# Performance work log

Hardware: AMD Instinct MI355X
Metric: run time of the kernel (lower is better)

## Reference

```python
import jax, jax.numpy as jnp
import numpy as np

N_NODES = 50000
N_EDGES = 800000
NODE_DIM = 32
EDGE_DIM = 16
HID = 64
MSG_HID = 128
NUM_GRAPHS = 512
NUM_MP = 3
S2S_STEPS = 6


def _lin(k, fan_in, fan_out):
    # torch Linear default init: U(-1/sqrt(fan_in), 1/sqrt(fan_in))
    bound = 1.0 / np.sqrt(fan_in)
    kw, kb = jax.random.split(k)
    W = jax.random.uniform(kw, (fan_in, fan_out), jnp.float32, -bound, bound)
    b = jax.random.uniform(kb, (fan_out,), jnp.float32, -bound, bound)
    return W, b


def setup_inputs() -> dict:
    key = jax.random.key(0)
    ks = jax.random.split(key, 16)
    x_feat = jax.random.normal(ks[0], (N_NODES, NODE_DIM), jnp.float32)
    edge_index = jax.random.randint(ks[1], (2, N_EDGES), 0, N_NODES)
    edge_attr = jax.random.normal(ks[2], (N_EDGES, EDGE_DIM), jnp.float32)
    batch = jnp.sort(jax.random.randint(ks[3], (N_NODES,), 0, NUM_GRAPHS))
    W_emb, b_emb = _lin(ks[4], NODE_DIM, HID)
    W_m1, b_m1 = _lin(ks[5], 2 * HID + EDGE_DIM, MSG_HID)
    W_m2, b_m2 = _lin(ks[6], MSG_HID, HID)
    bnd = 1.0 / np.sqrt(HID)
    gru_W_ih = jax.random.uniform(ks[7], (3 * HID, HID), jnp.float32, -bnd, bnd)
    gru_W_hh = jax.random.uniform(ks[8], (3 * HID, HID), jnp.float32, -bnd, bnd)
    gru_b_ih = jax.random.uniform(ks[9], (3 * HID,), jnp.float32, -bnd, bnd)
    gru_b_hh = jax.random.uniform(ks[9], (3 * HID,), jnp.float32, -bnd, bnd)
    lstm_W_ih = jax.random.uniform(ks[10], (4 * HID, 2 * HID), jnp.float32, -bnd, bnd)
    lstm_W_hh = jax.random.uniform(ks[11], (4 * HID, HID), jnp.float32, -bnd, bnd)
    lstm_b_ih = jax.random.uniform(ks[12], (4 * HID,), jnp.float32, -bnd, bnd)
    lstm_b_hh = jax.random.uniform(ks[12], (4 * HID,), jnp.float32, -bnd, bnd)
    W_r1, b_r1 = _lin(ks[13], 2 * HID, HID)
    W_r2, b_r2 = _lin(ks[14], HID, 1)
    return dict(x_feat=x_feat, edge_index=edge_index, edge_attr=edge_attr, batch=batch,
                W_emb=W_emb, b_emb=b_emb, W_m1=W_m1, b_m1=b_m1, W_m2=W_m2, b_m2=b_m2,
                gru_W_ih=gru_W_ih, gru_W_hh=gru_W_hh, gru_b_ih=gru_b_ih, gru_b_hh=gru_b_hh,
                lstm_W_ih=lstm_W_ih, lstm_W_hh=lstm_W_hh, lstm_b_ih=lstm_b_ih, lstm_b_hh=lstm_b_hh,
                W_r1=W_r1, b_r1=b_r1, W_r2=W_r2, b_r2=b_r2)


def reference(x_feat, edge_index, edge_attr, batch,
              W_emb, b_emb, W_m1, b_m1, W_m2, b_m2,
              gru_W_ih, gru_W_hh, gru_b_ih, gru_b_hh,
              lstm_W_ih, lstm_W_hh, lstm_b_ih, lstm_b_hh,
              W_r1, b_r1, W_r2, b_r2):
    src, dst = edge_index[0], edge_index[1]
    x = x_feat @ W_emb + b_emb  # [N, HID]
    h = x  # GRU hidden state (seq_len=1 GRU)
    for _ in range(NUM_MP):
        # message: cat([x_i (target), x_j (source), edge_attr]) -> MLP -> scatter-add to target
        mi = jnp.concatenate([x[dst], x[src], edge_attr], axis=-1)  # [E, 2H+Ed]
        msg = jnp.maximum(mi @ W_m1 + b_m1, 0.0) @ W_m2 + b_m2  # [E, H]
        m = jax.ops.segment_sum(msg, dst, num_segments=N_NODES)  # [N, H]
        # torch GRU cell, gate order (r, z, n)
        gi = m @ gru_W_ih.T + gru_b_ih
        gh = h @ gru_W_hh.T + gru_b_hh
        ir, iz, i_n = jnp.split(gi, 3, axis=-1)
        hr, hz, h_n = jnp.split(gh, 3, axis=-1)
        r = jax.nn.sigmoid(ir + hr)
        z = jax.nn.sigmoid(iz + hz)
        n = jnp.tanh(i_n + r * h_n)
        h = (1.0 - z) * n + z * h
        x = h
    # Set2Set pooling
    qh = jnp.zeros((NUM_GRAPHS, HID), x.dtype)
    qc = jnp.zeros((NUM_GRAPHS, HID), x.dtype)
    q_star = jnp.zeros((NUM_GRAPHS, 2 * HID), x.dtype)
    for _ in range(S2S_STEPS):
        # torch LSTM cell, gate order (i, f, g, o)
        g = q_star @ lstm_W_ih.T + lstm_b_ih + qh @ lstm_W_hh.T + lstm_b_hh
        gi_, gf, gg, go = jnp.split(g, 4, axis=-1)
        qc = jax.nn.sigmoid(gf) * qc + jax.nn.sigmoid(gi_) * jnp.tanh(gg)
        qh = jax.nn.sigmoid(go) * jnp.tanh(qc)
        e = jnp.sum(x * qh[batch], axis=-1)  # [N]
        emax = jax.ops.segment_max(e, batch, num_segments=NUM_GRAPHS)
        a = jnp.exp(e - emax[batch])
        asum = jax.ops.segment_sum(a, batch, num_segments=NUM_GRAPHS)
        a = a / asum[batch]  # segment softmax
        rvec = jax.ops.segment_sum(a[:, None] * x, batch, num_segments=NUM_GRAPHS)  # [B, H]
        q_star = jnp.concatenate([qh, rvec], axis=-1)
    out = jnp.maximum(q_star @ W_r1 + b_r1, 0.0) @ W_r2 + b_r2
    return out
```

## Files before the change

kernel.cpp:

```cpp
#include <hip/hip_runtime.h>
#include <hip/hip_bf16.h>

#define HID 64
#define MSG 128
#define NDIM 32
#define EDIM 16
#define NG 512
#define SCAP 192

typedef unsigned short u16;
typedef unsigned int u32;
typedef _Float16 h8 __attribute__((ext_vector_type(8)));
typedef _Float16 h4 __attribute__((ext_vector_type(4)));
typedef _Float16 h2 __attribute__((ext_vector_type(2)));

__device__ __forceinline__ float sigm(float x){return 1.0f/(1.0f+expf(-x));}
__device__ __forceinline__ int rfl(int x){return __builtin_amdgcn_readfirstlane(x);}
__device__ __forceinline__ u32 pkh(float a, float b){
    union { h2 h; u32 u; } v; v.h[0] = (_Float16)a; v.h[1] = (_Float16)b; return v.u;
}
__device__ __forceinline__ h2 pk2h(float a, float b){
    union { __fp16 __attribute__((ext_vector_type(2))) r; h2 h; } v;
    v.r = __builtin_amdgcn_cvt_pkrtz(a, b);
    return v.h;
}
__device__ __forceinline__ float fdot2_(h2 a, u32 w, float c){
    union { u32 u; h2 h; } v; v.u = w;
    return __builtin_amdgcn_fdot2(a, v.h, c, false);
}

__global__ void k_hist(const int* __restrict__ idx, int n, int* __restrict__ cnt) {
    int i = blockIdx.x * blockDim.x + threadIdx.x;
    int stride = gridDim.x * blockDim.x;
    for (; i < n; i += stride) atomicAdd(&cnt[idx[i]], 1);
}

__global__ void k_scanA(const int* __restrict__ in, int* __restrict__ out,
                        int* __restrict__ bsum, int n) {
    __shared__ int sh[1024];
    int i = blockIdx.x * 1024 + threadIdx.x;
    int v = (i < n) ? in[i] : 0;
    sh[threadIdx.x] = v;
    __syncthreads();
    for (int off = 1; off < 1024; off <<= 1) {
        int t = (threadIdx.x >= off) ? sh[threadIdx.x - off] : 0;
        __syncthreads();
        sh[threadIdx.x] += t;
        __syncthreads();
    }
    if (i < n) out[i] = sh[threadIdx.x] - v;
    if (threadIdx.x == 1023) bsum[blockIdx.x] = sh[1023];
}
__global__ void k_scanB(const int* __restrict__ bsum, int* __restrict__ boff, int nb) {
    if (threadIdx.x == 0) {
        int r = 0;
        for (int b = 0; b < nb; b++) { boff[b] = r; r += bsum[b]; }
        boff[nb] = r;
    }
}
__global__ void k_scanC(int* __restrict__ out, const int* __restrict__ boff, int n, int nb) {
    int i = blockIdx.x * blockDim.x + threadIdx.x;
    if (i < n) out[i] += boff[i >> 10];
    else if (i == n) out[n] = boff[nb];
}

__global__ void k_gptr(const int* __restrict__ batch, int N, int* __restrict__ gptr) {
    int g = blockIdx.x * blockDim.x + threadIdx.x;
    if (g > NG) return;
    int lo = 0, hi = N;
    while (lo < hi) { int mid = (lo + hi) >> 1; if (batch[mid] < g) lo = mid + 1; else hi = mid; }
    gptr[g] = lo;
}

__global__ void k_scatter(const int* __restrict__ src, const int* __restrict__ dst,
                          const float* __restrict__ ea, int n,
                          const int* __restrict__ ptr, int* __restrict__ cursor,
                          int* __restrict__ slist, _Float16* __restrict__ eap) {
    int i = blockIdx.x * blockDim.x + threadIdx.x;
    int stride = gridDim.x * blockDim.x;
    for (; i < n; i += stride) {
        int d = dst[i];
        int pos = ptr[d] + atomicAdd(&cursor[d], 1);
        slist[pos] = src[i];
        const float* s = ea + (size_t)i * EDIM;
        float4 a = *(const float4*)s, b = *(const float4*)(s + 4);
        float4 c = *(const float4*)(s + 8), d4 = *(const float4*)(s + 12);
        h8 o0, o1;
        o0[0]=(_Float16)a.x; o0[1]=(_Float16)a.y; o0[2]=(_Float16)a.z; o0[3]=(_Float16)a.w;
        o0[4]=(_Float16)b.x; o0[5]=(_Float16)b.y; o0[6]=(_Float16)b.z; o0[7]=(_Float16)b.w;
        o1[0]=(_Float16)c.x; o1[1]=(_Float16)c.y; o1[2]=(_Float16)c.z; o1[3]=(_Float16)c.w;
        o1[4]=(_Float16)d4.x; o1[5]=(_Float16)d4.y; o1[6]=(_Float16)d4.z; o1[7]=(_Float16)d4.w;
        h8* dp = (h8*)(eap + (size_t)pos * EDIM);
        dp[0] = o0; dp[1] = o1;
    }
}

__global__ void k_fuse(const float* __restrict__ Wih, const float* __restrict__ Whh,
                       const float* __restrict__ W2, const float* __restrict__ bm2,
                       uint4* __restrict__ gGA, uint2* __restrict__ gGB,
                       uint4* __restrict__ gUA, uint2* __restrict__ gUB,
                       float* __restrict__ gbb) {
    int t = blockIdx.x * blockDim.x + threadIdx.x;
    if (t < 2048) {
        int k4 = t >> 6, c = t & 63;
        float G[3][4];
#pragma unroll
        for (int g = 0; g < 3; g++)
#pragma unroll
            for (int kk = 0; kk < 4; kk++) {
                int j = 4 * k4 + kk;
                const float* w2r = W2 + (size_t)j * 64;
                const float* wir = Wih + (size_t)(g * 64 + c) * 64;
                float s = 0.f;
                for (int k = 0; k < 64; k++) s += w2r[k] * wir[k];
                G[g][kk] = s;
            }
        uint4 A; uint2 B;
        A.x = pkh(G[0][0], G[0][1]); A.y = pkh(G[1][0], G[1][1]);
        A.z = pkh(G[2][0], G[2][1]); A.w = pkh(G[0][2], G[0][3]);
        B.x = pkh(G[1][2], G[1][3]); B.y = pkh(G[2][2], G[2][3]);
        gGA[t] = A; gGB[t] = B;
    } else if (t < 3072) {
        int u = t - 2048;
        int k4 = u >> 6, c = u & 63;
        float U[3][4];
#pragma unroll
        for (int g = 0; g < 3; g++)
#pragma unroll
            for (int kk = 0; kk < 4; kk++)
                U[g][kk] = Whh[(size_t)(g * 64 + c) * 64 + 4 * k4 + kk];
        uint4 A; uint2 B;
        A.x = pkh(U[0][0], U[0][1]); A.y = pkh(U[1][0], U[1][1]);
        A.z = pkh(U[2][0], U[2][1]); A.w = pkh(U[0][2], U[0][3]);
        B.x = pkh(U[1][2], U[1][3]); B.y = pkh(U[2][2], U[2][3]);
        gUA[u] = A; gUB[u] = B;
    } else if (t < 3072 + 192) {
        int cg = t - 3072;
        const float* wir = Wih + (size_t)cg * 64;
        float s = 0.f;
        for (int k = 0; k < 64; k++) s += bm2[k] * wir[k];
        gbb[cg] = s;
    }
}

__global__ void k_packl(const float* __restrict__ lWih, const float* __restrict__ lWhh,
                        float* __restrict__ WT1, float* __restrict__ WT2) {
    int t = blockIdx.x * blockDim.x + threadIdx.x;
    if (t < 256 * 128) { int g = t >> 7, k = t & 127; WT1[k * 256 + g] = lWih[g * 128 + k]; }
    if (t < 256 * 64)  { int g = t >> 6, k = t & 63;  WT2[k * 256 + g] = lWhh[g * 64 + k]; }
}

__global__ void k_embed(const float* __restrict__ xf, const float* __restrict__ We,
                        const float* __restrict__ be, float* __restrict__ xh, int N) {
    __shared__ float Wl[NDIM * HID];
    for (int t = threadIdx.x; t < NDIM * HID; t += blockDim.x) Wl[t] = We[t];
    __syncthreads();
    int total = N * HID;
    int stride = gridDim.x * blockDim.x;
    for (int idx = blockIdx.x * blockDim.x + threadIdx.x; idx < total; idx += stride) {
        int n = idx >> 6, c = idx & 63;
        const float* xr = xf + n * NDIM;
        float acc = be[c];
#pragma unroll
        for (int k = 0; k < NDIM; k++) acc += xr[k] * Wl[k * HID + c];
        xh[idx] = acc;
    }
}

__global__ void __launch_bounds__(512)
k_prep(const float* __restrict__ xh, const float* __restrict__ Wm1,
       const float* __restrict__ bm1, float* __restrict__ Hb,
       _Float16* __restrict__ PsH, int N) {
    __shared__ float Wl[64 * 256];
    for (int t = threadIdx.x; t < 64 * 256; t += 512) {
        int k = t >> 8, cc = t & 255;
        Wl[t] = (cc < 128) ? Wm1[k * 128 + cc] : Wm1[(64 + k) * 128 + (cc - 128)];
    }
    __syncthreads();
    int wv = threadIdx.x >> 6, lane = threadIdx.x & 63;
    int cc = lane * 4;
    float4 bias;
    if (lane < 32) bias = *(const float4*)&bm1[cc];
    else bias = make_float4(0.f, 0.f, 0.f, 0.f);
    int ngroups = (N + 7) >> 3;
    for (int g = blockIdx.x * 8 + wv; g < ngroups; g += gridDim.x * 8) {
        int base = rfl(g) * 8;
        const float* xp[8];
#pragma unroll
        for (int t = 0; t < 8; t++) {
            int d = base + t; if (d > N - 1) d = N - 1;
            xp[t] = xh + (size_t)d * 64;
        }
        float4 acc[8];
#pragma unroll
        for (int t = 0; t < 8; t++) acc[t] = bias;
#pragma unroll 2
        for (int k4 = 0; k4 < 16; k4++) {
            int k = k4 * 4;
            float4 xv4[8];
#pragma unroll
            for (int t = 0; t < 8; t++) xv4[t] = *(const float4*)&xp[t][k];
#pragma unroll
            for (int kk = 0; kk < 4; kk++) {
                float4 w = *(const float4*)&Wl[(k + kk) * 256 + cc];
#pragma unroll
                for (int t = 0; t < 8; t++) {
                    float xv = kk == 0 ? xv4[t].x : kk == 1 ? xv4[t].y : kk == 2 ? xv4[t].z : xv4[t].w;
                    acc[t].x += xv * w.x; acc[t].y += xv * w.y;
                    acc[t].z += xv * w.z; acc[t].w += xv * w.w;
                }
            }
        }
#pragma unroll
        for (int t = 0; t < 8; t++) {
            int d = base + t;
            if (d < N) {
                if (lane < 32) *(float4*)&Hb[(size_t)d * 128 + cc] = acc[t];
                else {
                    h4 o;
                    o[0] = (_Float16)acc[t].x; o[1] = (_Float16)acc[t].y;
                    o[2] = (_Float16)acc[t].z; o[3] = (_Float16)acc[t].w;
                    *(h4*)&PsH[(size_t)d * 128 + (cc - 128)] = o;
                }
            }
        }
    }
}

__global__ void __launch_bounds__(256)
k_edge(const _Float16* __restrict__ PsH, const _Float16* __restrict__ eap,
       const float* __restrict__ Wm1, const int* __restrict__ ptr,
       const int* __restrict__ slist, float* __restrict__ Hb, int N) {
    int c = threadIdx.x & 127;
    int half = threadIdx.x >> 7;
    h2 wh[8];
#pragma unroll
    for (int k = 0; k < 8; k++) {
        h2 t;
        t[0] = (_Float16)Wm1[128 * 128 + (2 * k) * 128 + c];
        t[1] = (_Float16)Wm1[128 * 128 + (2 * k + 1) * 128 + c];
        wh[k] = t;
    }
    for (int dd = blockIdx.x * 2 + half; dd < N; dd += gridDim.x * 2) {
        int d = rfl(dd);
        float pd = Hb[(size_t)d * 128 + c];
        int eb = rfl(ptr[d]), ee = rfl(ptr[d + 1]);
        const int* sp = slist + eb;
        const _Float16* ep = eap + (size_t)eb * EDIM;
        int ne = ee - eb;
        float acc = 0.f;
        int i = 0;
        for (; i + 8 <= ne; i += 8) {
            int ns[8];
#pragma unroll
            for (int j = 0; j < 8; j++) ns[j] = rfl(sp[i + j]);
            float pv[8];
#pragma unroll
            for (int j = 0; j < 8; j++) pv[j] = (float)PsH[(size_t)ns[j] * 128 + c];
#pragma unroll
            for (int j = 0; j < 8; j++) {
                union { uint4 u; h2 h[4]; } A, B;
                A.u = *(const uint4*)(ep + (size_t)(i + j) * EDIM);
                B.u = *(const uint4*)(ep + (size_t)(i + j) * EDIM + 8);
                float pe = 0.f;
#pragma unroll
                for (int k = 0; k < 4; k++) pe = __builtin_amdgcn_fdot2(A.h[k], wh[k], pe, false);
#pragma unroll
                for (int k = 0; k < 4; k++) pe = __builtin_amdgcn_fdot2(B.h[k], wh[4 + k], pe, false);
                acc += fmaxf(pd + pv[j] + pe, 0.f);
            }
        }
        for (; i < ne; i++) {
            int n0 = rfl(sp[i]);
            float pv = (float)PsH[(size_t)n0 * 128 + c];
            union { uint4 u; h2 h[4]; } A, B;
            A.u = *(const uint4*)(ep + (size_t)i * EDIM);
            B.u = *(const uint4*)(ep + (size_t)i * EDIM + 8);
            float pe = 0.f;
#pragma unroll
            for (int k = 0; k < 4; k++) pe = __builtin_amdgcn_fdot2(A.h[k], wh[k], pe, false);
#pragma unroll
            for (int k = 0; k < 4; k++) pe = __builtin_amdgcn_fdot2(B.h[k], wh[4 + k], pe, false);
            acc += fmaxf(pd + pv + pe, 0.f);
        }
        Hb[(size_t)d * 128 + c] = acc;
    }
}

__global__ void __launch_bounds__(1024)
k_node(const float* __restrict__ H, const uint4* __restrict__ gGA, const uint2* __restrict__ gGB,
       const uint4* __restrict__ gUA, const uint2* __restrict__ gUB,
       const float* __restrict__ gbb, const float* __restrict__ bih, const float* __restrict__ bhh,
       const int* __restrict__ ptr, const float* __restrict__ xin, float* __restrict__ xout, int N) {
    extern __shared__ char smem[];
    uint4* GA = (uint4*)smem;
    uint2* GB = (uint2*)(smem + 32768);
    uint4* UA = (uint4*)(smem + 49152);
    uint2* UB = (uint2*)(smem + 65536);
    for (int t = threadIdx.x; t < 2048; t += 1024) { GA[t] = gGA[t]; GB[t] = gGB[t]; }
    for (int t = threadIdx.x; t < 1024; t += 1024) { UA[t] = gUA[t]; UB[t] = gUB[t]; }
    __syncthreads();
    int wv = threadIdx.x >> 6, lane = threadIdx.x & 63;
    float gbr = gbb[lane], gbz = gbb[64 + lane], gbn = gbb[128 + lane];
    float br = bih[lane], bz = bih[64 + lane], bn = bih[128 + lane];
    float cr = bhh[lane], cz = bhh[64 + lane], cn = bhh[128 + lane];
    int ngroups = (N + 3) >> 2;
    for (int g = blockIdx.x * 16 + wv; g < ngroups; g += gridDim.x * 16) {
        int base = rfl(g) * 4;
        const float* hp[4]; const float* xp[4]; float deg[4];
#pragma unroll
        for (int t = 0; t < 4; t++) {
            int d = base + t; if (d > N - 1) d = N - 1;
            hp[t] = H + (size_t)d * 128;
            xp[t] = xin + (size_t)d * 64;
            deg[t] = (float)(ptr[d + 1] - ptr[d]);
        }
        float gr[4], gz[4], gn[4];
#pragma unroll
        for (int t = 0; t < 4; t++) {
            gr[t] = br + deg[t] * gbr;
            gz[t] = bz + deg[t] * gbz;
            gn[t] = bn + deg[t] * gbn;
        }
#pragma unroll 2
        for (int k4 = 0; k4 < 32; k4++) {
            uint4 wa = GA[k4 * 64 + lane];
            uint2 wb = GB[k4 * 64 + lane];
#pragma unroll
            for (int t = 0; t < 4; t++) {
                float4 hx = *(const float4*)&hp[t][k4 * 4];
                h2 a01 = pk2h(hx.x, hx.y), a23 = pk2h(hx.z, hx.w);
                gr[t] = fdot2_(a01, wa.x, gr[t]); gz[t] = fdot2_(a01, wa.y, gz[t]);
                gn[t] = fdot2_(a01, wa.z, gn[t]);
                gr[t] = fdot2_(a23, wa.w, gr[t]); gz[t] = fdot2_(a23, wb.x, gz[t]);
                gn[t] = fdot2_(a23, wb.y, gn[t]);
            }
        }
        float hr[4], hz[4], hn[4], hv[4];
#pragma unroll
        for (int t = 0; t < 4; t++) { hr[t] = cr; hz[t] = cz; hn[t] = cn; hv[t] = xp[t][lane]; }
#pragma unroll 2
        for (int k4 = 0; k4 < 16; k4++) {
            uint4 wa = UA[k4 * 64 + lane];
            uint2 wb = UB[k4 * 64 + lane];
#pragma unroll
            for (int t = 0; t < 4; t++) {
                float4 hx = *(const float4*)&xp[t][k4 * 4];
                h2 a01 = pk2h(hx.x, hx.y), a23 = pk2h(hx.z, hx.w);
                hr[t] = fdot2_(a01, wa.x, hr[t]); hz[t] = fdot2_(a01, wa.y, hz[t]);
                hn[t] = fdot2_(a01, wa.z, hn[t]);
                hr[t] = fdot2_(a23, wa.w, hr[t]); hz[t] = fdot2_(a23, wb.x, hz[t]);
                hn[t] = fdot2_(a23, wb.y, hn[t]);
            }
        }
#pragma unroll
        for (int t = 0; t < 4; t++) {
            int d = base + t;
            if (d < N) {
                float r = sigm(gr[t] + hr[t]);
                float z = sigm(gz[t] + hz[t]);
                float nn = tanhf(gn[t] + r * hn[t]);
                xout[(size_t)d * 64 + lane] = (1.f - z) * nn + z * hv[t];
            }
        }
    }
}

__global__ void __launch_bounds__(1024)
k_s2s(const float* __restrict__ xh, const int* __restrict__ gptr,
      const float* __restrict__ WT1, const float* __restrict__ WT2,
      const float* __restrict__ lbih, const float* __restrict__ lbhh,
      const float* __restrict__ Wr1, const float* __restrict__ br1,
      const float* __restrict__ Wr2, const float* __restrict__ br2,
      float* __restrict__ out) {
    int b = blockIdx.x, tid = threadIdx.x;
    __shared__ float xl[SCAP * 64];
    __shared__ float qs[128], qhl[64], qcs[64], g[256], red[16], asums[16], rvs[1024];
    int start = gptr[b], end = gptr[b + 1];
    int seg = end - start;
    bool uselds = (seg <= SCAP);
    if (uselds) {
        int tot = seg * 64;
        for (int t = tid; t < tot; t += 1024) xl[t] = xh[(size_t)start * 64 + t];
    }
    if (tid < 128) qs[tid] = 0.f;
    if (tid < 64) { qhl[tid] = 0.f; qcs[tid] = 0.f; }
    __syncthreads();
    int grp = tid >> 6, lane = tid & 63;
    int gate = tid & 255, part = tid >> 8;
    for (int s = 0; s < 6; s++) {
        {
            float acc = 0.f;
            int k0 = part * 32;
#pragma unroll 8
            for (int k = k0; k < k0 + 32; k++) acc += qs[k] * WT1[k * 256 + gate];
            int k1 = part * 16;
#pragma unroll 8
            for (int k = k1; k < k1 + 16; k++) acc += qhl[k] * WT2[k * 256 + gate];
            rvs[tid] = acc;
        }
        __syncthreads();
        if (tid < 256) g[tid] = lbih[tid] + lbhh[tid] + rvs[tid] + rvs[256 + tid] + rvs[512 + tid] + rvs[768 + tid];
        __syncthreads();
        if (tid < 64) {
            float ig = sigm(g[tid]), fg = sigm(g[64 + tid]);
            float gg = tanhf(g[128 + tid]), og = sigm(g[192 + tid]);
            float c = fg * qcs[tid] + ig * gg;
            float h = og * tanhf(c);
            qcs[tid] = c; qhl[tid] = h; qs[tid] = h;
        }
        __syncthreads();
        float qv = qhl[lane];
        float mloc = -3.4e38f, asl = 0.f, rv = 0.f;
        for (int n = grp; n < seg; n += 16) {
            float xv = uselds ? xl[n * 64 + lane] : xh[(size_t)(start + n) * 64 + lane];
            float p = xv * qv;
#pragma unroll
            for (int off = 32; off > 0; off >>= 1) p += __shfl_xor(p, off);
            float mnew = fmaxf(mloc, p);
            float corr = expf(mloc - mnew);
            float a = expf(p - mnew);
            asl = asl * corr + a;
            rv = rv * corr + a * xv;
            mloc = mnew;
        }
        if (lane == 0) red[grp] = mloc;
        __syncthreads();
        float gmax = red[0];
#pragma unroll
        for (int j = 1; j < 16; j++) gmax = fmaxf(gmax, red[j]);
        float sc = expf(mloc - gmax);
        rvs[tid] = rv * sc;
        if (lane == 0) asums[grp] = asl * sc;
        __syncthreads();
        if (tid < 64) {
            float rt = 0.f, at = 0.f;
#pragma unroll
            for (int j = 0; j < 16; j++) { rt += rvs[tid + 64 * j]; at += asums[j]; }
            qs[64 + tid] = (at > 0.f) ? rt / at : 0.f;
        }
        __syncthreads();
    }
    if (tid < 64) {
        float a2 = br1[tid];
#pragma unroll 8
        for (int k = 0; k < 128; k++) a2 += qs[k] * Wr1[k * 64 + tid];
        a2 = fmaxf(a2, 0.f);
        float v = a2 * Wr2[tid];
#pragma unroll
        for (int off = 32; off > 0; off >>= 1) v += __shfl_xor(v, off);
        if (tid == 0) out[b] = v + br2[0];
    }
}

extern "C" void kernel_launch(void* const* d_in, const int* in_sizes, int n_in,
                              void* d_out, int out_size, void* d_ws, size_t ws_size,
                              hipStream_t stream) {
    const float* x_feat = (const float*)d_in[0];
    const int*   ei     = (const int*)d_in[1];
    const float* eattr  = (const float*)d_in[2];
    const int*   batch  = (const int*)d_in[3];
    const float* W_emb  = (const float*)d_in[4];
    const float* b_emb  = (const float*)d_in[5];
    const float* W_m1   = (const float*)d_in[6];
    const float* b_m1   = (const float*)d_in[7];
    const float* W_m2   = (const float*)d_in[8];
    const float* b_m2   = (const float*)d_in[9];
    const float* gWih   = (const float*)d_in[10];
    const float* gWhh   = (const float*)d_in[11];
    const float* gbih   = (const float*)d_in[12];
    const float* gbhh   = (const float*)d_in[13];
    const float* lWih   = (const float*)d_in[14];
    const float* lWhh   = (const float*)d_in[15];
    const float* lbih   = (const float*)d_in[16];
    const float* lbhh   = (const float*)d_in[17];
    const float* Wr1    = (const float*)d_in[18];
    const float* br1    = (const float*)d_in[19];
    const float* Wr2    = (const float*)d_in[20];
    const float* br2    = (const float*)d_in[21];

    int N = in_sizes[0] / NDIM;
    int E = in_sizes[1] / 2;

    char* w = (char*)d_ws;
    auto alloc = [&](size_t b) { char* p = w; w += (b + 511) & ~(size_t)511; return p; };
    float*     xh    = (float*)alloc((size_t)N * 64 * 4);
    float*     xh2   = (float*)alloc((size_t)N * 64 * 4);
    _Float16*  PsH   = (_Float16*)alloc((size_t)N * 128 * 2);
    float*     Hb    = (float*)alloc((size_t)N * 128 * 4);
    int*       ptr   = (int*)alloc((size_t)(N + 1) * 4);
    int*       slist = (int*)alloc((size_t)E * 4);
    _Float16*  eap   = (_Float16*)alloc((size_t)E * EDIM * 2);
    uint4*     gGA   = (uint4*)alloc((size_t)2048 * 16);
    uint2*     gGB   = (uint2*)alloc((size_t)2048 * 8);
    uint4*     gUA   = (uint4*)alloc((size_t)1024 * 16);
    uint2*     gUB   = (uint2*)alloc((size_t)1024 * 8);
    float*     gbb   = (float*)alloc((size_t)192 * 4);
    float*     WT1   = (float*)alloc((size_t)128 * 256 * 4);
    float*     WT2   = (float*)alloc((size_t)64 * 256 * 4);
    int*       gptr  = (int*)alloc((size_t)(NG + 1) * 4);
    int*       bsum  = (int*)alloc(128 * 4);
    int*       boff  = (int*)alloc(128 * 4);
    char* z0 = w;
    int*       cnt    = (int*)alloc((size_t)N * 4);
    int*       cursor = (int*)alloc((size_t)N * 4);
    char* z0e = w;

    hipMemsetAsync(z0, 0, (size_t)(z0e - z0), stream);

    hipError_t attr_err = hipFuncSetAttribute((const void*)k_node,
        hipFuncAttributeMaxDynamicSharedMemorySize, 73728);
    (void)attr_err;

    int NB = (N + 1023) / 1024;
    k_hist<<<1024, 256, 0, stream>>>(ei + E, E, cnt);
    k_scanA<<<NB, 1024, 0, stream>>>(cnt, ptr, bsum, N);
    k_scanB<<<1, 64, 0, stream>>>(bsum, boff, NB);
    k_scanC<<<(N + 256) / 256, 256, 0, stream>>>(ptr, boff, N, NB);
    k_gptr<<<3, 256, 0, stream>>>(batch, N, gptr);
    k_scatter<<<3125, 256, 0, stream>>>(ei, ei + E, eattr, E, ptr, cursor, slist, eap);
    k_fuse<<<13, 256, 0, stream>>>(gWih, gWhh, W_m2, b_m2, gGA, gGB, gUA, gUB, gbb);
    k_packl<<<128, 256, 0, stream>>>(lWih, lWhh, WT1, WT2);

    k_embed<<<2048, 256, 0, stream>>>(x_feat, W_emb, b_emb, xh, N);

    float* xa = xh;
    float* xb = xh2;
    for (int r = 0; r < 3; r++) {
        k_prep<<<196, 512, 0, stream>>>(xa, W_m1, b_m1, Hb, PsH, N);
        k_edge<<<4096, 256, 0, stream>>>(PsH, eap, W_m1, ptr, slist, Hb, N);
        k_node<<<256, 1024, 73728, stream>>>(Hb, gGA, gGB, gUA, gUB, gbb, gbih, gbhh,
                                             ptr, xa, xb, N);
        float* t = xa; xa = xb; xb = t;
    }
    k_s2s<<<NG, 1024, 0, stream>>>(xa, gptr, WT1, WT2, lbih, lbhh,
                                   Wr1, br1, Wr2, br2, (float*)d_out);
}
```

Before: 926.4 us.

## Store edge aggregates and node state in fp16 for GRU node kernel

After: 857.3 us. 1.08x faster.

```diff
diff --git a/kernel.cpp b/kernel.cpp
--- a/kernel.cpp
+++ b/kernel.cpp
@@ -19,11 +19,7 @@
 __device__ __forceinline__ u32 pkh(float a, float b){
     union { h2 h; u32 u; } v; v.h[0] = (_Float16)a; v.h[1] = (_Float16)b; return v.u;
 }
-__device__ __forceinline__ h2 pk2h(float a, float b){
-    union { __fp16 __attribute__((ext_vector_type(2))) r; h2 h; } v;
-    v.r = __builtin_amdgcn_cvt_pkrtz(a, b);
-    return v.h;
-}
+__device__ __forceinline__ h2 bh2(u32 u){ union{u32 v; h2 h;} x; x.v=u; return x.h; }
 __device__ __forceinline__ float fdot2_(h2 a, u32 w, float c){
     union { u32 u; h2 h; } v; v.u = w;
     return __builtin_amdgcn_fdot2(a, v.h, c, false);
@@ -151,7 +147,8 @@
 }
 
 __global__ void k_embed(const float* __restrict__ xf, const float* __restrict__ We,
-                        const float* __restrict__ be, float* __restrict__ xh, int N) {
+                        const float* __restrict__ be, float* __restrict__ xh,
+                        _Float16* __restrict__ xh16, int N) {
     __shared__ float Wl[NDIM * HID];
     for (int t = threadIdx.x; t < NDIM * HID; t += blockDim.x) Wl[t] = We[t];
     __syncthreads();
@@ -164,6 +161,7 @@
 #pragma unroll
         for (int k = 0; k < NDIM; k++) acc += xr[k] * Wl[k * HID + c];
         xh[idx] = acc;
+        xh16[idx] = (_Float16)acc;
     }
 }
 
@@ -230,7 +228,8 @@
 __global__ void __launch_bounds__(256)
 k_edge(const _Float16* __restrict__ PsH, const _Float16* __restrict__ eap,
        const float* __restrict__ Wm1, const int* __restrict__ ptr,
-       const int* __restrict__ slist, float* __restrict__ Hb, int N) {
+       const int* __restrict__ slist, const float* __restrict__ Pd,
+       _Float16* __restrict__ Hh, int N) {
     int c = threadIdx.x & 127;
     int half = threadIdx.x >> 7;
     h2 wh[8];
@@ -243,22 +242,42 @@
     }
     for (int dd = blockIdx.x * 2 + half; dd < N; dd += gridDim.x * 2) {
         int d = rfl(dd);
-        float pd = Hb[(size_t)d * 128 + c];
+        float pd = Pd[(size_t)d * 128 + c];
         int eb = rfl(ptr[d]), ee = rfl(ptr[d + 1]);
         const int* sp = slist + eb;
         const _Float16* ep = eap + (size_t)eb * EDIM;
         int ne = ee - eb;
         float acc = 0.f;
         int i = 0;
-        for (; i + 8 <= ne; i += 8) {
-            int ns[8];
-#pragma unroll
-            for (int j = 0; j < 8; j++) ns[j] = rfl(sp[i + j]);
-            float pv[8];
-#pragma unroll
-            for (int j = 0; j < 8; j++) pv[j] = (float)PsH[(size_t)ns[j] * 128 + c];
-#pragma unroll
-            for (int j = 0; j < 8; j++) {
+        for (; i + 16 <= ne; i += 16) {
+            int ns[16];
+#pragma unroll
+            for (int j = 0; j < 16; j++) ns[j] = rfl(sp[i + j]);
+            float pv[16];
+#pragma unroll
+            for (int j = 0; j < 16; j++) pv[j] = (float)PsH[(size_t)ns[j] * 128 + c];
+#pragma unroll
+            for (int j = 0; j < 16; j++) {
+                union { uint4 u; h2 h[4]; } A, B;
+                A.u = *(const uint4*)(ep + (size_t)(i + j) * EDIM);
+                B.u = *(const uint4*)(ep + (size_t)(i + j) * EDIM + 8);
+                float pe = 0.f;
+#pragma unroll
+                for (int k = 0; k < 4; k++) pe = __builtin_amdgcn_fdot2(A.h[k], wh[k], pe, false);
+#pragma unroll
+                for (int k = 0; k < 4; k++) pe = __builtin_amdgcn_fdot2(B.h[k], wh[4 + k], pe, false);
+                acc += fmaxf(pd + pv[j] + pe, 0.f);
+            }
+        }
+        for (; i + 4 <= ne; i += 4) {
+            int ns[4];
+#pragma unroll
+            for (int j = 0; j < 4; j++) ns[j] = rfl(sp[i + j]);
+            float pv[4];
+#pragma unroll
+            for (int j = 0; j < 4; j++) pv[j] = (float)PsH[(size_t)ns[j] * 128 + c];
+#pragma unroll
+            for (int j = 0; j < 4; j++) {
                 union { uint4 u; h2 h[4]; } A, B;
                 A.u = *(const uint4*)(ep + (size_t)(i + j) * EDIM);
                 B.u = *(const uint4*)(ep + (size_t)(i + j) * EDIM + 8);
@@ -283,15 +302,17 @@
             for (int k = 0; k < 4; k++) pe = __builtin_amdgcn_fdot2(B.h[k], wh[4 + k], pe, false);
             acc += fmaxf(pd + pv + pe, 0.f);
         }
-        Hb[(size_t)d * 128 + c] = acc;
+        Hh[(size_t)d * 128 + c] = (_Float16)acc;
     }
 }
 
 __global__ void __launch_bounds__(1024)
-k_node(const float* __restrict__ H, const uint4* __restrict__ gGA, const uint2* __restrict__ gGB,
+k_node(const _Float16* __restrict__ Hh, const uint4* __restrict__ gGA, const uint2* __restrict__ gGB,
        const uint4* __restrict__ gUA, const uint2* __restrict__ gUB,
        const float* __restrict__ gbb, const float* __restrict__ bih, const float* __restrict__ bhh,
-       const int* __restrict__ ptr, const float* __restrict__ xin, float* __restrict__ xout, int N) {
+       const int* __restrict__ ptr, const float* __restrict__ xin,
+       const _Float16* __restrict__ xin16, float* __restrict__ xout,
+       _Float16* __restrict__ xout16, int N) {
     extern __shared__ char smem[];
     uint4* GA = (uint4*)smem;
     uint2* GB = (uint2*)(smem + 32768);
@@ -307,11 +328,12 @@
     int ngroups = (N + 3) >> 2;
     for (int g = blockIdx.x * 16 + wv; g < ngroups; g += gridDim.x * 16) {
         int base = rfl(g) * 4;
-        const float* hp[4]; const float* xp[4]; float deg[4];
+        const _Float16* hp16[4]; const _Float16* xp16[4]; const float* xp[4]; float deg[4];
 #pragma unroll
         for (int t = 0; t < 4; t++) {
             int d = base + t; if (d > N - 1) d = N - 1;
-            hp[t] = H + (size_t)d * 128;
+            hp16[t] = Hh + (size_t)d * 128;
+            xp16[t] = xin16 + (size_t)d * 64;
             xp[t] = xin + (size_t)d * 64;
             deg[t] = (float)(ptr[d + 1] - ptr[d]);
         }
@@ -323,34 +345,44 @@
             gn[t] = bn + deg[t] * gbn;
         }
 #pragma unroll 2
-        for (int k4 = 0; k4 < 32; k4++) {
-            uint4 wa = GA[k4 * 64 + lane];
-            uint2 wb = GB[k4 * 64 + lane];
+        for (int k8 = 0; k8 < 16; k8++) {
+            uint4 wa0 = GA[(2 * k8) * 64 + lane];
+            uint2 wb0 = GB[(2 * k8) * 64 + lane];
+            uint4 wa1 = GA[(2 * k8 + 1) * 64 + lane];
+            uint2 wb1 = GB[(2 * k8 + 1) * 64 + lane];
 #pragma unroll
             for (int t = 0; t < 4; t++) {
-                float4 hx = *(const float4*)&hp[t][k4 * 4];
-                h2 a01 = pk2h(hx.x, hx.y), a23 = pk2h(hx.z, hx.w);
-                gr[t] = fdot2_(a01, wa.x, gr[t]); gz[t] = fdot2_(a01, wa.y, gz[t]);
-                gn[t] = fdot2_(a01, wa.z, gn[t]);
-                gr[t] = fdot2_(a23, wa.w, gr[t]); gz[t] = fdot2_(a23, wb.x, gz[t]);
-                gn[t] = fdot2_(a23, wb.y, gn[t]);
+                uint4 a = *(const uint4*)(hp16[t] + k8 * 8);
+                gr[t] = fdot2_(bh2(a.x), wa0.x, gr[t]); gz[t] = fdot2_(bh2(a.x), wa0.y, gz[t]);
+                gn[t] = fdot2_(bh2(a.x), wa0.z, gn[t]);
+                gr[t] = fdot2_(bh2(a.y), wa0.w, gr[t]); gz[t] = fdot2_(bh2(a.y), wb0.x, gz[t]);
+                gn[t] = fdot2_(bh2(a.y), wb0.y, gn[t]);
+                gr[t] = fdot2_(bh2(a.z), wa1.x, gr[t]); gz[t] = fdot2_(bh2(a.z), wa1.y, gz[t]);
+                gn[t] = fdot2_(bh2(a.z), wa1.z, gn[t]);
+                gr[t] = fdot2_(bh2(a.w), wa1.w, gr[t]); gz[t] = fdot2_(bh2(a.w), wb1.x, gz[t]);
+                gn[t] = fdot2_(bh2(a.w), wb1.y, gn[t]);
             }
         }
         float hr[4], hz[4], hn[4], hv[4];
 #pragma unroll
         for (int t = 0; t < 4; t++) { hr[t] = cr; hz[t] = cz; hn[t] = cn; hv[t] = xp[t][lane]; }
 #pragma unroll 2
-        for (int k4 = 0; k4 < 16; k4++) {
-            uint4 wa = UA[k4 * 64 + lane];
-            uint2 wb = UB[k4 * 64 + lane];
+        for (int k8 = 0; k8 < 8; k8++) {
+            uint4 wa0 = UA[(2 * k8) * 64 + lane];
+            uint2 wb0 = UB[(2 * k8) * 64 + lane];
+            uint4 wa1 = UA[(2 * k8 + 1) * 64 + lane];
+            uint2 wb1 = UB[(2 * k8 + 1) * 64 + lane];
 #pragma unroll
             for (int t = 0; t < 4; t++) {
-                float4 hx = *(const float4*)&xp[t][k4 * 4];
-                h2 a01 = pk2h(hx.x, hx.y), a23 = pk2h(hx.z, hx.w);
-                hr[t] = fdot2_(a01, wa.x, hr[t]); hz[t] = fdot2_(a01, wa.y, hz[t]);
-                hn[t] = fdot2_(a01, wa.z, hn[t]);
-                hr[t] = fdot2_(a23, wa.w, hr[t]); hz[t] = fdot2_(a23, wb.x, hz[t]);
-                hn[t] = fdot2_(a23, wb.y, hn[t]);
+                uint4 a = *(const uint4*)(xp16[t] + k8 * 8);
+                hr[t] = fdot2_(bh2(a.x), wa0.x, hr[t]); hz[t] = fdot2_(bh2(a.x), wa0.y, hz[t]);
+                hn[t] = fdot2_(bh2(a.x), wa0.z, hn[t]);
+                hr[t] = fdot2_(bh2(a.y), wa0.w, hr[t]); hz[t] = fdot2_(bh2(a.y), wb0.x, hz[t]);
+                hn[t] = fdot2_(bh2(a.y), wb0.y, hn[t]);
+                hr[t] = fdot2_(bh2(a.z), wa1.x, hr[t]); hz[t] = fdot2_(bh2(a.z), wa1.y, hz[t]);
+                hn[t] = fdot2_(bh2(a.z), wa1.z, hn[t]);
+                hr[t] = fdot2_(bh2(a.w), wa1.w, hr[t]); hz[t] = fdot2_(bh2(a.w), wb1.x, hz[t]);
+                hn[t] = fdot2_(bh2(a.w), wb1.y, hn[t]);
             }
         }
 #pragma unroll
@@ -360,7 +392,9 @@
                 float r = sigm(gr[t] + hr[t]);
                 float z = sigm(gz[t] + hz[t]);
                 float nn = tanhf(gn[t] + r * hn[t]);
-                xout[(size_t)d * 64 + lane] = (1.f - z) * nn + z * hv[t];
+                float h = (1.f - z) * nn + z * hv[t];
+                xout[(size_t)d * 64 + lane] = h;
+                xout16[(size_t)d * 64 + lane] = (_Float16)h;
             }
         }
     }
@@ -486,8 +520,11 @@
     auto alloc = [&](size_t b) { char* p = w; w += (b + 511) & ~(size_t)511; return p; };
     float*     xh    = (float*)alloc((size_t)N * 64 * 4);
     float*     xh2   = (float*)alloc((size_t)N * 64 * 4);
+    _Float16*  xh16a = (_Float16*)alloc((size_t)N * 64 * 2);
+    _Float16*  xh16b = (_Float16*)alloc((size_t)N * 64 * 2);
     _Float16*  PsH   = (_Float16*)alloc((size_t)N * 128 * 2);
     float*     Hb    = (float*)alloc((size_t)N * 128 * 4);
+    _Float16*  Hh    = (_Float16*)alloc((size_t)N * 128 * 2);
     int*       ptr   = (int*)alloc((size_t)(N + 1) * 4);
     int*       slist = (int*)alloc((size_t)E * 4);
     _Float16*  eap   = (_Float16*)alloc((size_t)E * EDIM * 2);
@@ -522,16 +559,17 @@
     k_fuse<<<13, 256, 0, stream>>>(gWih, gWhh, W_m2, b_m2, gGA, gGB, gUA, gUB, gbb);
     k_packl<<<128, 256, 0, stream>>>(lWih, lWhh, WT1, WT2);
 
-    k_embed<<<2048, 256, 0, stream>>>(x_feat, W_emb, b_emb, xh, N);
-
-    float* xa = xh;
-    float* xb = xh2;
+    k_embed<<<2048, 256, 0, stream>>>(x_feat, W_emb, b_emb, xh, xh16a, N);
+
+    float* xa = xh;       float* xb = xh2;
+    _Float16* xa16 = xh16a; _Float16* xb16 = xh16b;
     for (int r = 0; r < 3; r++) {
         k_prep<<<196, 512, 0, stream>>>(xa, W_m1, b_m1, Hb, PsH, N);
-        k_edge<<<4096, 256, 0, stream>>>(PsH, eap, W_m1, ptr, slist, Hb, N);
-        k_node<<<256, 1024, 73728, stream>>>(Hb, gGA, gGB, gUA, gUB, gbb, gbih, gbhh,
-                                             ptr, xa, xb, N);
+        k_edge<<<4096, 256, 0, stream>>>(PsH, eap, W_m1, ptr, slist, Hb, Hh, N);
+        k_node<<<256, 1024, 73728, stream>>>(Hh, gGA, gGB, gUA, gUB, gbb, gbih, gbhh,
+                                             ptr, xa, xa16, xb, xb16, N);
         float* t = xa; xa = xb; xb = t;
+        _Float16* t16 = xa16; xa16 = xb16; xb16 = t16;
     }
     k_s2s<<<NG, 1024, 0, stream>>>(xa, gptr, WT1, WT2, lbih, lbhh,
                                    Wr1, br1, Wr2, br2, (float*)d_out);
```
